# Optimization experiments

Hardware: AMD Instinct MI355X
Metric: run time of the kernel (lower is better)

The kernel has to match this reference:

```python
import jax, jax.numpy as jnp
import numpy as np

D_MODEL = 1024
N_HEADS = 16
D_K = D_MODEL // N_HEADS
SIGMA = 1.0
NUM_ITERS = 3
PAD_POS = 10000.0


def setup_inputs() -> dict:
    rng = jax.random.key(0)
    ks = jax.random.split(rng, 16)
    B, Lq, Lk = 8, 512, 512
    s = 1.0 / np.sqrt(D_MODEL).astype(np.float32)
    return {
        "query": jax.random.normal(ks[0], (B, Lq, D_MODEL), jnp.float32),
        "key": jax.random.normal(ks[1], (B, Lk, D_MODEL), jnp.float32),
        "value": jax.random.normal(ks[2], (B, Lk, D_MODEL), jnp.float32),
        "query_lengths": jax.random.randint(ks[3], (B,), 2, Lq),
        "key_lengths": jax.random.randint(ks[4], (B,), 2, Lk),
        "Wq": jax.random.normal(ks[5], (D_MODEL, D_MODEL), jnp.float32) * s,
        "bq": jnp.zeros((D_MODEL,), jnp.float32),
        "Wk": jax.random.normal(ks[6], (D_MODEL, D_MODEL), jnp.float32) * s,
        "bk": jnp.zeros((D_MODEL,), jnp.float32),
        "Wv": jax.random.normal(ks[7], (D_MODEL, D_MODEL), jnp.float32) * s,
        "bv": jnp.zeros((D_MODEL,), jnp.float32),
        "Wo": jax.random.normal(ks[8], (D_MODEL, D_MODEL), jnp.float32) * s,
        "bo": jnp.zeros((D_MODEL,), jnp.float32),
        "pos_scale": jnp.ones((1,), jnp.float32),
        "pos_bias": jnp.zeros((1,), jnp.float32),
    }


def _init_positions(lengths, max_len, scale, bias):
    # vectorized tcr_pep init: linspace(-L/2, L/2, L) per row, pad -> 10000
    j = jnp.arange(max_len, dtype=jnp.float32)[None, :]          # [1, L]
    L = lengths.astype(jnp.float32)[:, None]                      # [B, 1]
    step = jnp.where(L > 1.0, L / (L - 1.0), 0.0)                 # linspace step
    pos = (-L / 2.0 + j * step) * scale + bias
    pad = jnp.arange(max_len)[None, :] >= lengths[:, None]
    return jnp.where(pad, PAD_POS, pos)


def _distance_attention(qp, kp):
    d2 = (qp[:, :, None] - kp[:, None, :]) ** 2                   # [B, Lq, Lk]
    attn = jnp.exp(-d2 / (2.0 * SIGMA * SIGMA))
    masked = (qp[:, :, None] >= 1000.0) | (kp[:, None, :] >= 1000.0)
    return jnp.where(masked, 0.0, attn)


def _update_positions(qp, kp, attn):
    qn = attn / jnp.clip(attn.sum(-1, keepdims=True), 1e-9)
    qp_new = jnp.einsum('bqk,bk->bq', qn, kp)
    at = attn.transpose(0, 2, 1)
    kn = at / jnp.clip(at.sum(-1, keepdims=True), 1e-9)
    kp_new = jnp.einsum('bkq,bq->bk', kn, qp)
    qp_new = jnp.where(qp >= 1000.0, PAD_POS, qp_new)
    kp_new = jnp.where(kp >= 1000.0, PAD_POS, kp_new)
    return qp_new, kp_new


def reference(query, key, value, query_lengths, key_lengths,
              Wq, bq, Wk, bk, Wv, bv, Wo, bo, pos_scale, pos_bias):
    B, Lq, _ = query.shape
    Lk = key.shape[1]

    def split_heads(x):
        return x.reshape(B, -1, N_HEADS, D_K).transpose(0, 2, 1, 3)  # [B,H,L,Dk]

    q = split_heads(query @ Wq.T + bq)
    k = split_heads(key @ Wk.T + bk)
    v = split_heads(value @ Wv.T + bv)

    qp = _init_positions(query_lengths, Lq, pos_scale, pos_bias)  # [B, Lq]
    kp = _init_positions(key_lengths, Lk, pos_scale, pos_bias)    # [B, Lk]

    scores = jnp.einsum('bhqd,bhkd->bhqk', q, k) / jnp.sqrt(jnp.float32(D_K))
    attn = jax.nn.softmax(scores, axis=-1)                        # [B,H,Lq,Lk]

    for _ in range(NUM_ITERS):
        da = _distance_attention(qp, kp)                          # [B,Lq,Lk]
        comb = attn * da[:, None, :, :]
        comb = comb / jnp.clip(comb.sum(-1, keepdims=True), 1e-9)
        qp, kp = _update_positions(qp, kp, da)
        attn = comb

    ctx = jnp.einsum('bhqk,bhkd->bhqd', attn, v)
    ctx = ctx.transpose(0, 2, 1, 3).reshape(B, Lq, D_MODEL)
    out = ctx @ Wo.T + bo
    return out, attn.mean(axis=1)
```

## Files before the change

kernel.cpp:

```cpp
#include <hip/hip_runtime.h>
#include <math.h>

#define B_  8
#define LQ  512
#define LK  512
#define DM  1024
#define NH  16
#define DK  64
constexpr float PADP = 10000.0f;

typedef short s16x8 __attribute__((ext_vector_type(8)));
typedef float f32x4 __attribute__((ext_vector_type(4)));

__device__ inline unsigned short f2b1(float f) {
    unsigned u = __float_as_uint(f);
    unsigned r = (u + 0x7fffu + ((u >> 16) & 1u)) >> 16;
    return (unsigned short)r;
}
__device__ inline float b2f1(unsigned short h) {
    return __uint_as_float(((unsigned)h) << 16);
}

__global__ __launch_bounds__(256) void f2b_all_kernel(
    const float* __restrict__ query, const float* __restrict__ key,
    const float* __restrict__ value,
    const float* __restrict__ Wq, const float* __restrict__ Wk,
    const float* __restrict__ Wv, const float* __restrict__ Wo,
    unsigned short* __restrict__ xq, unsigned short* __restrict__ xk,
    unsigned short* __restrict__ xv,
    unsigned short* __restrict__ wqb, unsigned short* __restrict__ wkb,
    unsigned short* __restrict__ wvb, unsigned short* __restrict__ wob)
{
    const int s = blockIdx.y;
    const float* src;
    unsigned short* dst;
    if (s < 4)       { src = query + ((size_t)s << 20);       dst = xq + ((size_t)s << 20); }
    else if (s < 8)  { src = key   + ((size_t)(s - 4) << 20); dst = xk + ((size_t)(s - 4) << 20); }
    else if (s < 12) { src = value + ((size_t)(s - 8) << 20); dst = xv + ((size_t)(s - 8) << 20); }
    else {
        const int w = s - 12;
        src = (w == 0) ? Wq : (w == 1) ? Wk : (w == 2) ? Wv : Wo;
        dst = (w == 0) ? wqb : (w == 1) ? wkb : (w == 2) ? wvb : wob;
    }
    const int i = blockIdx.x * 256 + threadIdx.x;
    const float4 v = *(const float4*)&src[(size_t)i * 4];
    ushort4 o;
    o.x = f2b1(v.x); o.y = f2b1(v.y); o.z = f2b1(v.z); o.w = f2b1(v.w);
    *(ushort4*)&dst[(size_t)i * 4] = o;
}

template <int PHASE>
__global__ __launch_bounds__(512) void daRow_kernel(
    const int* __restrict__ qlen, const int* __restrict__ klen,
    const float* __restrict__ pscale, const float* __restrict__ pbias,
    float* __restrict__ posQ,
    const float* __restrict__ posKin, float* __restrict__ posKout,
    const float* __restrict__ rsIn, const float* __restrict__ rdIn,
    const float* __restrict__ colSIn, const float* __restrict__ colDIn,
    float* __restrict__ rsOut, float* __restrict__ rdOut,
    float* __restrict__ colSOut, float* __restrict__ colDOut,
    unsigned short* __restrict__ Dplane)
{
    constexpr int NCH = 16, QC = LQ / NCH;
    __shared__ float kpl[LK];
    __shared__ float csp[8][LK], cdp[8][LK];
    const int chunk = blockIdx.x, b = blockIdx.y;
    const int t = threadIdx.x, w = t >> 6, lane = t & 63;

    float scale = 0.0f, bias = 0.0f;
    if (PHASE == 0) { scale = pscale[0]; bias = pbias[0]; }

    if (PHASE == 0) {
        const int kl = klen[b];
        const float Lf = (float)kl;
        const float step = (Lf > 1.0f) ? Lf / (Lf - 1.0f) : 0.0f;
        const float pos = (-Lf * 0.5f + (float)t * step) * scale + bias;
        const float kv = (t >= kl) ? PADP : pos;
        kpl[t] = kv;
        if (chunk == 0) posKout[b * LK + t] = kv;
    } else {
        float colsum = 0.0f, coldot = 0.0f;
#pragma unroll
        for (int c = 0; c < NCH; ++c) {
            colsum += colSIn[((size_t)b * NCH + c) * LK + t];
            coldot += colDIn[((size_t)b * NCH + c) * LK + t];
        }
        const float prev = posKin[b * LK + t];
        const float kv = (prev >= 1000.0f) ? PADP : coldot / fmaxf(colsum, 1e-9f);
        kpl[t] = kv;
        if (PHASE == 1 && chunk == 0) posKout[b * LK + t] = kv;
    }
    __syncthreads();

    float cs[8] = {0,0,0,0,0,0,0,0}, cd[8] = {0,0,0,0,0,0,0,0};
    unsigned short* Dbb = Dplane + (size_t)b * LQ * LK;

    for (int qi = chunk * QC + w; qi < chunk * QC + QC; qi += 8) {
        float qpv;
        if (PHASE == 0) {
            const int ql = qlen[b];
            const float Lf = (float)ql;
            const float step = (Lf > 1.0f) ? Lf / (Lf - 1.0f) : 0.0f;
            qpv = (qi >= ql) ? PADP : (-Lf * 0.5f + (float)qi * step) * scale + bias;
            if (lane == 0) posQ[b * LQ + qi] = qpv;
        } else {
            const float prev = posQ[b * LQ + qi];
            qpv = (prev >= 1000.0f) ? PADP
                : rdIn[b * LQ + qi] / fmaxf(rsIn[b * LQ + qi], 1e-9f);
            if (PHASE == 1 && lane == 0) posQ[b * LQ + qi] = qpv;
        }
        const bool qpad = (qpv >= 1000.0f);
        float rsum = 0.0f, rdot = 0.0f;
#pragma unroll
        for (int c = 0; c < 8; ++c) {
            const int k = lane + 64 * c;
            const float kpv = kpl[k];
            const float d = qpv - kpv;
            float e = (qpad || (kpv >= 1000.0f)) ? 0.0f : __expf(-0.5f * d * d);
            if (PHASE < 2) { rsum += e; rdot += e * kpv; cs[c] += e; cd[c] += e * qpv; }
            Dbb[(size_t)qi * LK + k] = f2b1(e);
        }
        if (PHASE < 2) {
#pragma unroll
            for (int o = 32; o > 0; o >>= 1) {
                rsum += __shfl_xor(rsum, o);
                rdot += __shfl_xor(rdot, o);
            }
            if (lane == 0) { rsOut[b * LQ + qi] = rsum; rdOut[b * LQ + qi] = rdot; }
        }
    }
    if (PHASE < 2) {
#pragma unroll
        for (int c = 0; c < 8; ++c) {
            csp[w][lane + 64 * c] = cs[c];
            cdp[w][lane + 64 * c] = cd[c];
        }
        __syncthreads();
        float s = 0.0f, dd = 0.0f;
        for (int ww = 0; ww < 8; ++ww) { s += csp[ww][t]; dd += cdp[ww][t]; }
        colSOut[((size_t)b * NCH + chunk) * LK + t] = s;
        colDOut[((size_t)b * NCH + chunk) * LK + t] = dd;
    }
}

__global__ __launch_bounds__(256) void transpose_bf16(
    const unsigned short* __restrict__ in, unsigned short* __restrict__ out,
    int Mn, int Nn)
{
    __shared__ unsigned short tile[64][65];
    const int m0 = blockIdx.y * 64, n0 = blockIdx.x * 64;
    const int t = threadIdx.x;
    const int r = t >> 3, c8 = (t & 7) * 8;
#pragma unroll
    for (int rr = 0; rr < 64; rr += 32) {
        const uint4 v = *(const uint4*)&in[(size_t)(m0 + r + rr) * Nn + n0 + c8];
        const unsigned short* pv = (const unsigned short*)&v;
#pragma unroll
        for (int j = 0; j < 8; ++j) tile[r + rr][c8 + j] = pv[j];
    }
    __syncthreads();
#pragma unroll
    for (int rr = 0; rr < 64; rr += 32) {
        unsigned short tmp[8];
#pragma unroll
        for (int j = 0; j < 8; ++j) tmp[j] = tile[c8 + j][r + rr];
        *(uint4*)&out[(size_t)(n0 + r + rr) * Mn + m0 + c8] = *(uint4*)tmp;
    }
}

template <bool OB>
__global__ __launch_bounds__(256) void gemm_bf16_nt(
    const unsigned short* __restrict__ A,
    const unsigned short* __restrict__ Bt,
    void* __restrict__ Cv,
    const float* __restrict__ bias,
    int M, int N, int K)
{
    __shared__ short As[64 * 32];
    __shared__ short Bs[128 * 32];
    const int m0 = blockIdx.y * 64, n0 = blockIdx.x * 128;
    const int t = threadIdx.x;
    const int wid = t >> 6, lane = t & 63;
    const int wr = wid >> 1, wc = wid & 1;
    const int lr = lane & 15, lk = (lane >> 4) * 8;

    f32x4 acc[2][4] = {};

    const int srow = lane >> 2;
    const int scol = (lane & 3) * 8;

    for (int kb = 0; kb < K; kb += 32) {
        __syncthreads();
        {
            const unsigned short* g = &A[(size_t)(m0 + wid * 16 + srow) * K + kb + scol];
            __builtin_amdgcn_global_load_lds((const unsigned*)g,
                (unsigned*)&As[(wid * 16) * 32], 16, 0, 0);
        }
#pragma unroll
        for (int u = 0; u < 2; ++u) {
            const unsigned short* g = &Bt[(size_t)(n0 + wid * 32 + u * 16 + srow) * K + kb + scol];
            __builtin_amdgcn_global_load_lds((const unsigned*)g,
                (unsigned*)&Bs[(wid * 32 + u * 16) * 32], 16, 0, 0);
        }
        __syncthreads();

        s16x8 af[2], bf[4];
#pragma unroll
        for (int i = 0; i < 2; ++i)
            af[i] = *(const s16x8*)&As[(wr * 32 + i * 16 + lr) * 32 + lk];
#pragma unroll
        for (int j = 0; j < 4; ++j)
            bf[j] = *(const s16x8*)&Bs[(wc * 64 + j * 16 + lr) * 32 + lk];
#pragma unroll
        for (int i = 0; i < 2; ++i)
#pragma unroll
            for (int j = 0; j < 4; ++j)
                acc[i][j] = __builtin_amdgcn_mfma_f32_16x16x32_bf16(
                    af[i], bf[j], acc[i][j], 0, 0, 0);
    }

    const int r0 = (lane >> 4) * 4;
#pragma unroll
    for (int i = 0; i < 2; ++i) {
        const int row = m0 + wr * 32 + i * 16 + r0;
#pragma unroll
        for (int j = 0; j < 4; ++j) {
            const int col = n0 + wc * 64 + j * 16 + lr;
            const float bvv = bias ? bias[col] : 0.0f;
#pragma unroll
            for (int r = 0; r < 4; ++r) {
                const float val = acc[i][j][r] + bvv;
                if (OB) ((unsigned short*)Cv)[(size_t)(row + r) * N + col] = f2b1(val);
                else    ((float*)Cv)[(size_t)(row + r) * N + col] = val;
            }
        }
    }
}

__global__ __launch_bounds__(512) void attn_fused(
    const unsigned short* __restrict__ Qb,
    const unsigned short* __restrict__ Kb,
    const unsigned short* __restrict__ D,
    unsigned short* __restrict__ Ab)
{
    constexpr int KP = 72;
    constexpr int SP = 520;
    __shared__ short pool[64 * SP];
    __shared__ float red[8][64];
    short* Qs = pool;
    short* Ks = pool + 4608;

    const int z = blockIdx.y;
    const int b = z >> 4, h = z & 15;
    const int q0 = blockIdx.x * 64;
    const int t = threadIdx.x;
    const int wid = t >> 6, lane = t & 63;
    const int lr = lane & 15, lkq = (lane >> 4) * 8;
    const int rbase = (lane >> 4) * 4;

    {
        const int row = t >> 3, seg = (t & 7) * 8;
        *(uint4*)&Qs[row * KP + seg] =
            *(const uint4*)&Qb[((size_t)(b * LQ + q0 + row)) * DM + h * DK + seg];
    }

    f32x4 acc[2][4][2] = {};

#pragma unroll
    for (int kh = 0; kh < 2; ++kh) {
        __syncthreads();
        {
            const int row = t >> 1, seg = (t & 1) * 32;
            const unsigned short* src =
                &Kb[((size_t)(b * LK + kh * 256 + row)) * DM + h * DK + seg];
#pragma unroll
            for (int s = 0; s < 4; ++s)
                *(uint4*)&Ks[row * KP + seg + s * 8] = *(const uint4*)(src + s * 8);
        }
        __syncthreads();

#pragma unroll
        for (int ks = 0; ks < 2; ++ks) {
            s16x8 af[4], bf[2];
#pragma unroll
            for (int i = 0; i < 4; ++i)
                af[i] = *(const s16x8*)&Qs[(i * 16 + lr) * KP + ks * 32 + lkq];
#pragma unroll
            for (int j = 0; j < 2; ++j)
                bf[j] = *(const s16x8*)&Ks[(wid * 32 + j * 16 + lr) * KP + ks * 32 + lkq];
#pragma unroll
            for (int i = 0; i < 4; ++i)
#pragma unroll
                for (int j = 0; j < 2; ++j)
                    acc[kh][i][j] = __builtin_amdgcn_mfma_f32_16x16x32_bf16(
                        af[i], bf[j], acc[kh][i][j], 0, 0, 0);
        }
    }

    float M[4][4];
#pragma unroll
    for (int i = 0; i < 4; ++i)
#pragma unroll
        for (int r = 0; r < 4; ++r) {
            float m = acc[0][i][0][r];
            m = fmaxf(m, acc[0][i][1][r]);
            m = fmaxf(m, acc[1][i][0][r]);
            m = fmaxf(m, acc[1][i][1][r]);
#pragma unroll
            for (int o = 1; o < 16; o <<= 1)
                m = fmaxf(m, __shfl_xor(m, o));
            M[i][r] = m;
        }
    __syncthreads();
    if (lr == 0) {
#pragma unroll
        for (int i = 0; i < 4; ++i)
#pragma unroll
            for (int r = 0; r < 4; ++r)
                red[wid][i * 16 + rbase + r] = M[i][r];
    }
    __syncthreads();
#pragma unroll
    for (int i = 0; i < 4; ++i)
#pragma unroll
        for (int r = 0; r < 4; ++r) {
            float m = red[0][i * 16 + rbase + r];
#pragma unroll
            for (int ww = 1; ww < 8; ++ww)
                m = fmaxf(m, red[ww][i * 16 + rbase + r]);
            M[i][r] = m;
        }

#pragma unroll
    for (int kh = 0; kh < 2; ++kh)
#pragma unroll
        for (int i = 0; i < 4; ++i)
#pragma unroll
            for (int j = 0; j < 2; ++j) {
                const int col = kh * 256 + wid * 32 + j * 16 + lr;
#pragma unroll
                for (int r = 0; r < 4; ++r) {
                    const int row = i * 16 + rbase + r;
                    const float e = __expf((acc[kh][i][j][r] - M[i][r]) * 0.125f);
                    pool[row * SP + col] = (short)f2b1(e);
                }
            }
    __syncthreads();

    for (int rr = wid * 8; rr < wid * 8 + 8; ++rr) {
        float v[8];
        {
            const uint4 ev = *(const uint4*)&pool[rr * SP + lane * 8];
            const unsigned short* pe = (const unsigned short*)&ev;
#pragma unroll
            for (int j = 0; j < 8; ++j) v[j] = b2f1(pe[j]);
        }
        float s = 0.0f;
#pragma unroll
        for (int j = 0; j < 8; ++j) s += v[j];
#pragma unroll
        for (int o = 32; o > 0; o >>= 1) s += __shfl_xor(s, o);
        const float invz = 1.0f / s;
#pragma unroll
        for (int j = 0; j < 8; ++j) v[j] *= invz;

#pragma unroll
        for (int it = 0; it < 3; ++it) {
            const uint4 dv = *(const uint4*)&D[
                (((size_t)it * B_ + b) * LQ + q0 + rr) * LK + lane * 8];
            const unsigned short* pd = (const unsigned short*)&dv;
            float s2 = 0.0f;
#pragma unroll
            for (int j = 0; j < 8; ++j) {
                v[j] *= b2f1(pd[j]);
                s2 += v[j];
            }
#pragma unroll
            for (int o = 32; o > 0; o >>= 1) s2 += __shfl_xor(s2, o);
            const float inv = 1.0f / fmaxf(s2, 1e-9f);
#pragma unroll
            for (int j = 0; j < 8; ++j) v[j] *= inv;
        }

        ushort4 u0, u1;
        u0.x = f2b1(v[0]); u0.y = f2b1(v[1]); u0.z = f2b1(v[2]); u0.w = f2b1(v[3]);
        u1.x = f2b1(v[4]); u1.y = f2b1(v[5]); u1.z = f2b1(v[6]); u1.w = f2b1(v[7]);
        unsigned short* arow = Ab + ((size_t)z * LQ + q0 + rr) * LK + lane * 8;
        *(ushort4*)&arow[0] = u0;
        *(ushort4*)&arow[4] = u1;
    }
}

__global__ __launch_bounds__(256) void meanB_kernel(
    const unsigned short* __restrict__ Ab, float* __restrict__ meanOut)
{
    const int b = blockIdx.x >> 9, q = blockIdx.x & 511;
    const int t = threadIdx.x;
    const int c0 = t * 2;
    float s0 = 0.0f, s1 = 0.0f;
#pragma unroll
    for (int h = 0; h < 16; ++h) {
        const unsigned short* row = Ab + (((size_t)(b * 16 + h)) * LQ + q) * LK;
        const unsigned v = *(const unsigned*)&row[c0];
        s0 += b2f1((unsigned short)(v & 0xffff));
        s1 += b2f1((unsigned short)(v >> 16));
    }
    float* o = meanOut + ((size_t)b * LQ + q) * LK + c0;
    o[0] = s0 * (1.0f / 16.0f);
    o[1] = s1 * (1.0f / 16.0f);
}

__global__ __launch_bounds__(256) void ctx_mfma(
    const unsigned short* __restrict__ Ab,
    const unsigned short* __restrict__ VbT,
    unsigned short* __restrict__ ctxb)
{
    constexpr int BKP = 72;
    __shared__ short As[64 * BKP];
    __shared__ short Bs[64 * BKP];
    const int z = blockIdx.z;
    const int b = z >> 4, h = z & 15;
    const int hcol = h * DK;
    const int q0 = blockIdx.y * 64;
    const int t = threadIdx.x;
    const int wid = t >> 6, lane = t & 63;
    const int wr = wid >> 1, wc = wid & 1;
    const int lr = lane & 15, lk = (lane >> 4) * 8;

    const unsigned short* Abase = Ab + ((size_t)z * LQ + q0) * LK;
    const unsigned short* Bbase = VbT + (size_t)hcol * (B_ * LK) + (size_t)b * LK;

    f32x4 acc[2][2] = {};
    const int srow = t >> 2, sseg = (t & 3) * 16;

    for (int kb = 0; kb < LK; kb += 64) {
        const uint4 a0 = *(const uint4*)&Abase[(size_t)srow * LK + kb + sseg];
        const uint4 a1 = *(const uint4*)&Abase[(size_t)srow * LK + kb + sseg + 8];
        const uint4 b0 = *(const uint4*)&Bbase[(size_t)srow * (B_ * LK) + kb + sseg];
        const uint4 b1 = *(const uint4*)&Bbase[(size_t)srow * (B_ * LK) + kb + sseg + 8];
        __syncthreads();
        *(uint4*)&As[srow * BKP + sseg] = a0;
        *(uint4*)&As[srow * BKP + sseg + 8] = a1;
        *(uint4*)&Bs[srow * BKP + sseg] = b0;
        *(uint4*)&Bs[srow * BKP + sseg + 8] = b1;
        __syncthreads();

#pragma unroll
        for (int kh = 0; kh < 2; ++kh) {
            s16x8 af[2], bf[2];
#pragma unroll
            for (int i = 0; i < 2; ++i)
                af[i] = *(const s16x8*)&As[(wr * 32 + i * 16 + lr) * BKP + kh * 32 + lk];
#pragma unroll
            for (int j = 0; j < 2; ++j)
                bf[j] = *(const s16x8*)&Bs[(wc * 32 + j * 16 + lr) * BKP + kh * 32 + lk];
#pragma unroll
            for (int i = 0; i < 2; ++i)
#pragma unroll
                for (int j = 0; j < 2; ++j)
                    acc[i][j] = __builtin_amdgcn_mfma_f32_16x16x32_bf16(
                        af[i], bf[j], acc[i][j], 0, 0, 0);
        }
    }

    const int r0 = (lane >> 4) * 4;
#pragma unroll
    for (int i = 0; i < 2; ++i) {
        const int row = b * LQ + q0 + wr * 32 + i * 16 + r0;
#pragma unroll
        for (int j = 0; j < 2; ++j) {
            const int col = hcol + wc * 32 + j * 16 + lr;
#pragma unroll
            for (int r = 0; r < 4; ++r)
                ctxb[(size_t)(row + r) * DM + col] = f2b1(acc[i][j][r]);
        }
    }
}

template <bool BT>
__global__ __launch_bounds__(256) void gemm64(
    const float* __restrict__ A, int lda, long aS1, long aS2,
    const float* __restrict__ Bm, int ldb, long bS1, long bS2,
    float* __restrict__ C, int ldc, long cS1, long cS2,
    const float* __restrict__ bias, int K, float alpha, int zshift)
{
    const int z = blockIdx.z;
    const long z1 = z >> zshift;
    const long z2 = z & ((1 << zshift) - 1);
    A  += z1 * aS1 + z2 * aS2;
    Bm += z1 * bS1 + z2 * bS2;
    C  += z1 * cS1 + z2 * cS2;

    const int m0 = blockIdx.y * 64, n0 = blockIdx.x * 64;
    __shared__ float As[32][68];
    __shared__ float Bs[32][68];
    const int t = threadIdx.x;
    const int ty = t >> 4, tx = t & 15;

    float acc[4][4];
#pragma unroll
    for (int i = 0; i < 4; ++i)
#pragma unroll
        for (int j = 0; j < 4; ++j) acc[i][j] = 0.0f;

    const int mA = t >> 3;
    const int kA = (t & 7) * 4;

    for (int kb = 0; kb < K; kb += 32) {
        {
            const float4 a0 = *(const float4*)&A[(size_t)(m0 + mA) * lda + kb + kA];
            const float4 a1 = *(const float4*)&A[(size_t)(m0 + mA + 32) * lda + kb + kA];
            As[kA + 0][mA] = a0.x; As[kA + 1][mA] = a0.y; As[kA + 2][mA] = a0.z; As[kA + 3][mA] = a0.w;
            As[kA + 0][mA + 32] = a1.x; As[kA + 1][mA + 32] = a1.y; As[kA + 2][mA + 32] = a1.z; As[kA + 3][mA + 32] = a1.w;
        }
        if (BT) {
            const float4 b0 = *(const float4*)&Bm[(size_t)(n0 + mA) * ldb + kb + kA];
            const float4 b1 = *(const float4*)&Bm[(size_t)(n0 + mA + 32) * ldb + kb + kA];
            Bs[kA + 0][mA] = b0.x; Bs[kA + 1][mA] = b0.y; Bs[kA + 2][mA] = b0.z; Bs[kA + 3][mA] = b0.w;
            Bs[kA + 0][mA + 32] = b1.x; Bs[kA + 1][mA + 32] = b1.y; Bs[kA + 2][mA + 32] = b1.z; Bs[kA + 3][mA + 32] = b1.w;
        } else {
            const int kB = t >> 4;
            const int nB = (t & 15) * 4;
            const float4 b0 = *(const float4*)&Bm[(size_t)(kb + kB) * ldb + n0 + nB];
            const float4 b1 = *(const float4*)&Bm[(size_t)(kb + kB + 16) * ldb + n0 + nB];
            *(float4*)&Bs[kB][nB] = b0;
            *(float4*)&Bs[kB + 16][nB] = b1;
        }
        __syncthreads();

#pragma unroll
        for (int kk = 0; kk < 32; ++kk) {
            const float4 av = *(const float4*)&As[kk][ty * 4];
            const float4 bv = *(const float4*)&Bs[kk][tx * 4];
            const float a[4] = {av.x, av.y, av.z, av.w};
            const float bb[4] = {bv.x, bv.y, bv.z, bv.w};
#pragma unroll
            for (int i = 0; i < 4; ++i)
#pragma unroll
                for (int j = 0; j < 4; ++j)
                    acc[i][j] = fmaf(a[i], bb[j], acc[i][j]);
        }
        __syncthreads();
    }

#pragma unroll
    for (int i = 0; i < 4; ++i) {
        const int row = m0 + ty * 4 + i;
        float4 o;
        o.x = acc[i][0] * alpha;
        o.y = acc[i][1] * alpha;
        o.z = acc[i][2] * alpha;
        o.w = acc[i][3] * alpha;
        if (bias) {
            o.x += bias[n0 + tx * 4 + 0];
            o.y += bias[n0 + tx * 4 + 1];
            o.z += bias[n0 + tx * 4 + 2];
            o.w += bias[n0 + tx * 4 + 3];
        }
        *(float4*)&C[(size_t)row * ldc + n0 + tx * 4] = o;
    }
}

template <bool BF16OUT>
__global__ __launch_bounds__(256) void softmaxP_kernel(
    float* __restrict__ S, const unsigned short* __restrict__ D,
    void* __restrict__ AOut, float* __restrict__ meanOut,
    int nheads, int accumulate)
{
    const int b = blockIdx.x >> 9, q = blockIdx.x & 511;
    const int t = threadIdx.x, w = t >> 6, lane = t & 63;
    __shared__ float Pl[3][LK];
    __shared__ float part[4][LK];
    const size_t NPB = (size_t)B_ * LQ * LK;
    const size_t rowoff = ((size_t)b * LQ + q) * LK;

    for (int i = t; i < LK; i += 256) {
        Pl[0][i] = b2f1(D[rowoff + i]);
        Pl[1][i] = b2f1(D[NPB + rowoff + i]);
        Pl[2][i] = b2f1(D[2 * NPB + rowoff + i]);
    }
    __syncthreads();

    float macc[8];
#pragma unroll
    for (int j = 0; j < 8; ++j) macc[j] = 0.0f;

    for (int h = w; h < nheads; h += 4) {
        const size_t roff = (((size_t)b * nheads + h) * LQ + q) * LK;
        const float* row = S + roff;
        float v[8];
        const float4 s0 = *(const float4*)&row[lane * 8];
        const float4 s1 = *(const float4*)&row[lane * 8 + 4];
        v[0] = s0.x; v[1] = s0.y; v[2] = s0.z; v[3] = s0.w;
        v[4] = s1.x; v[5] = s1.y; v[6] = s1.z; v[7] = s1.w;
        float mx = v[0];
#pragma unroll
        for (int j = 1; j < 8; ++j) mx = fmaxf(mx, v[j]);
#pragma unroll
        for (int o = 32; o > 0; o >>= 1) mx = fmaxf(mx, __shfl_xor(mx, o));
        float zz = 0.0f;
#pragma unroll
        for (int j = 0; j < 8; ++j) { v[j] = __expf(v[j] - mx); zz += v[j]; }
#pragma unroll
        for (int o = 32; o > 0; o >>= 1) zz += __shfl_xor(zz, o);
        const float invz = 1.0f / zz;
#pragma unroll
        for (int j = 0; j < 8; ++j) v[j] *= invz;

#pragma unroll
        for (int it = 0; it < 3; ++it) {
            float s = 0.0f;
#pragma unroll
            for (int j = 0; j < 8; ++j) {
                v[j] *= Pl[it][lane * 8 + j];
                s += v[j];
            }
#pragma unroll
            for (int o = 32; o > 0; o >>= 1) s += __shfl_xor(s, o);
            const float inv = 1.0f / fmaxf(s, 1e-9f);
#pragma unroll
            for (int j = 0; j < 8; ++j) v[j] *= inv;
        }

#pragma unroll
        for (int j = 0; j < 8; ++j) macc[j] += v[j];

        if (BF16OUT) {
            unsigned short* arow = (unsigned short*)AOut + roff;
            ushort4 u0, u1;
            u0.x = f2b1(v[0]); u0.y = f2b1(v[1]); u0.z = f2b1(v[2]); u0.w = f2b1(v[3]);
            u1.x = f2b1(v[4]); u1.y = f2b1(v[5]); u1.z = f2b1(v[6]); u1.w = f2b1(v[7]);
            *(ushort4*)&arow[lane * 8] = u0;
            *(ushort4*)&arow[lane * 8 + 4] = u1;
        } else {
            float* arow = (float*)AOut + roff;
            *(float4*)&arow[lane * 8] = make_float4(v[0], v[1], v[2], v[3]);
            *(float4*)&arow[lane * 8 + 4] = make_float4(v[4], v[5], v[6], v[7]);
        }
    }

    *(float4*)&part[w][lane * 8] = make_float4(macc[0], macc[1], macc[2], macc[3]);
    *(float4*)&part[w][lane * 8 + 4] = make_float4(macc[4], macc[5], macc[6], macc[7]);
    __syncthreads();

    for (int i = t; i < LK; i += 256) {
        const float m = (part[0][i] + part[1][i] + part[2][i] + part[3][i]) * (1.0f / 16.0f);
        const size_t oi = ((size_t)b * LQ + q) * LK + i;
        meanOut[oi] = accumulate ? (meanOut[oi] + m) : m;
    }
}

extern "C" void kernel_launch(void* const* d_in, const int* in_sizes, int n_in,
                              void* d_out, int out_size, void* d_ws, size_t ws_size,
                              hipStream_t stream)
{
    const float* query  = (const float*)d_in[0];
    const float* key    = (const float*)d_in[1];
    const float* value  = (const float*)d_in[2];
    const int*   qlen   = (const int*)d_in[3];
    const int*   klen   = (const int*)d_in[4];
    const float* Wq     = (const float*)d_in[5];
    const float* bq     = (const float*)d_in[6];
    const float* Wk     = (const float*)d_in[7];
    const float* bk     = (const float*)d_in[8];
    const float* Wv     = (const float*)d_in[9];
    const float* bv     = (const float*)d_in[10];
    const float* Wo     = (const float*)d_in[11];
    const float* bo     = (const float*)d_in[12];
    const float* pscale = (const float*)d_in[13];
    const float* pbias  = (const float*)d_in[14];

    float* out     = (float*)d_out;
    float* meanOut = out + (size_t)B_ * LQ * DM;

    const size_t NQKV = (size_t)B_ * LQ * DM;
    const size_t NP   = (size_t)B_ * LQ * LK;
    const size_t NW   = (size_t)DM * DM;
    const size_t NS   = (size_t)B_ * NH * LQ * LK;
    const size_t NPOS = (size_t)B_ * LQ;
    const size_t NCOL = (size_t)B_ * 16 * LK;

    unsigned short* Dbuf = (unsigned short*)d_ws;
    float* posQ  = (float*)(Dbuf + 3 * NP);
    float* posK1 = posQ + NPOS;
    float* posK2 = posK1 + NPOS;
    float* rs1   = posK2 + NPOS;
    float* rd1   = rs1 + NPOS;
    float* rs2   = rd1 + NPOS;
    float* rd2   = rs2 + NPOS;
    float* colS1 = rd2 + NPOS;
    float* colD1 = colS1 + NCOL;
    float* colS2 = colD1 + NCOL;
    float* colD2 = colS2 + NCOL;
    float* fend  = colD2 + NCOL;
    unsigned short* Qb   = (unsigned short*)fend;
    unsigned short* Kb   = Qb + NQKV;
    unsigned short* Vb   = Kb + NQKV;
    unsigned short* VbT  = Vb + NQKV;
    unsigned short* ctxb = VbT + NQKV;
    unsigned short* wqb  = ctxb + NQKV;
    unsigned short* wkb  = wqb + NW;
    unsigned short* wvb  = wkb + NW;
    unsigned short* wob  = wvb + NW;
    unsigned short* Ab   = wob + NW;
    unsigned short* xq = Ab;
    unsigned short* xk = xq + NQKV;
    unsigned short* xv = xk + NQKV;

    const size_t need_full = (size_t)((char*)(Ab + NS) - (char*)d_ws);

    if (ws_size >= need_full) {
        dim3 gDa(16, B_);
        daRow_kernel<0><<<gDa, 512, 0, stream>>>(qlen, klen, pscale, pbias,
            posQ, nullptr, posK1,
            nullptr, nullptr, nullptr, nullptr,
            rs1, rd1, colS1, colD1, Dbuf);
        daRow_kernel<1><<<gDa, 512, 0, stream>>>(qlen, klen, pscale, pbias,
            posQ, posK1, posK2,
            rs1, rd1, colS1, colD1,
            rs2, rd2, colS2, colD2, Dbuf + NP);
        daRow_kernel<2><<<gDa, 512, 0, stream>>>(qlen, klen, pscale, pbias,
            posQ, posK2, nullptr,
            rs2, rd2, colS2, colD2,
            nullptr, nullptr, nullptr, nullptr, Dbuf + 2 * NP);

        dim3 gF(1024, 16);
        f2b_all_kernel<<<gF, 256, 0, stream>>>(query, key, value, Wq, Wk, Wv, Wo,
                                               xq, xk, xv, wqb, wkb, wvb, wob);

        dim3 gP(DM / 128, (B_ * LQ) / 64);
        gemm_bf16_nt<true><<<gP, 256, 0, stream>>>(xq, wqb, Qb, bq, B_ * LQ, DM, DM);
        gemm_bf16_nt<true><<<gP, 256, 0, stream>>>(xk, wkb, Kb, bk, B_ * LQ, DM, DM);
        gemm_bf16_nt<true><<<gP, 256, 0, stream>>>(xv, wvb, Vb, bv, B_ * LQ, DM, DM);

        dim3 gT(DM / 64, (B_ * LK) / 64);
        transpose_bf16<<<gT, 256, 0, stream>>>(Vb, VbT, B_ * LK, DM);

        dim3 gA(LQ / 64, B_ * NH);
        attn_fused<<<gA, 512, 0, stream>>>(Qb, Kb, Dbuf, Ab);

        meanB_kernel<<<B_ * LQ, 256, 0, stream>>>(Ab, meanOut);

        dim3 gC(1, LQ / 64, B_ * NH);
        ctx_mfma<<<gC, 256, 0, stream>>>(Ab, VbT, ctxb);

        gemm_bf16_nt<false><<<gP, 256, 0, stream>>>(ctxb, wob, out, bo, B_ * LQ, DM, DM);
        return;
    }

    float* qbuf = (float*)d_ws;
    float* kbuf = qbuf + NQKV;
    float* vbuf = kbuf + NQKV;
    unsigned short* Dfb = (unsigned short*)(vbuf + NQKV);
    float* Sfb  = (float*)(Dfb + 3 * NP);
    float* ctxbuf = Sfb + NP;
    float* pQ  = ctxbuf + NQKV;
    float* pK1 = pQ + NPOS;
    float* pK2 = pK1 + NPOS;
    float* frs1 = pK2 + NPOS;
    float* frd1 = frs1 + NPOS;
    float* frs2 = frd1 + NPOS;
    float* frd2 = frs2 + NPOS;
    float* fcS1 = frd2 + NPOS;
    float* fcD1 = fcS1 + NCOL;
    float* fcS2 = fcD1 + NCOL;
    float* fcD2 = fcS2 + NCOL;

    dim3 gDa(16, B_);
    daRow_kernel<0><<<gDa, 512, 0, stream>>>(qlen, klen, pscale, pbias,
        pQ, nullptr, pK1, nullptr, nullptr, nullptr, nullptr,
        frs1, frd1, fcS1, fcD1, Dfb);
    daRow_kernel<1><<<gDa, 512, 0, stream>>>(qlen, klen, pscale, pbias,
        pQ, pK1, pK2, frs1, frd1, fcS1, fcD1,
        frs2, frd2, fcS2, fcD2, Dfb + NP);
    daRow_kernel<2><<<gDa, 512, 0, stream>>>(qlen, klen, pscale, pbias,
        pQ, pK2, nullptr, frs2, frd2, fcS2, fcD2,
        nullptr, nullptr, nullptr, nullptr, Dfb + 2 * NP);

    dim3 gProj(DM / 64, (B_ * LQ) / 64, 1);
    gemm64<true><<<gProj, 256, 0, stream>>>(query, DM, 0, 0, Wq, DM, 0, 0,
                                            qbuf, DM, 0, 0, bq, DM, 1.0f, 0);
    gemm64<true><<<gProj, 256, 0, stream>>>(key, DM, 0, 0, Wk, DM, 0, 0,
                                            kbuf, DM, 0, 0, bk, DM, 1.0f, 0);
    gemm64<true><<<gProj, 256, 0, stream>>>(value, DM, 0, 0, Wv, DM, 0, 0,
                                            vbuf, DM, 0, 0, bv, DM, 1.0f, 0);
    for (int h = 0; h < NH; ++h) {
        dim3 gS2(LK / 64, LQ / 64, B_);
        gemm64<true><<<gS2, 256, 0, stream>>>(
            qbuf + h * DK, DM, (long)LQ * DM, 0,
            kbuf + h * DK, DM, (long)LK * DM, 0,
            Sfb, LK, (long)LQ * LK, 0,
            nullptr, DK, 0.125f, 0);
        softmaxP_kernel<false><<<B_ * LQ, 256, 0, stream>>>(Sfb, Dfb, Sfb, meanOut, 1, h > 0 ? 1 : 0);
        dim3 gC2(1, LQ / 64, B_);
        gemm64<false><<<gC2, 256, 0, stream>>>(
            Sfb, LK, (long)LQ * LK, 0,
            vbuf + h * DK, DM, (long)LK * DM, 0,
            ctxbuf + h * DK, DM, (long)LQ * DM, 0,
            nullptr, LK, 1.0f, 0);
    }
    dim3 gO(DM / 64, (B_ * LQ) / 64, 1);
    gemm64<true><<<gO, 256, 0, stream>>>(ctxbuf, DM, 0, 0, Wo, DM, 0, 0,
                                         out, DM, 0, 0, bo, DM, 1.0f, 0);
}
```

Baseline: 217.6 us.

## Split attention block into two 32-row halves to halve LDS and accumulators

The fused attention kernel now handles its 64 query rows as two sequential 32-row halves. K is streamed in four 128-row chunks instead of two 256-row chunks, and the shared pool and reduction buffers shrink by half. The aim is to cut LDS use and accumulator registers per block so more blocks fit on each CU and occupancy rises. In exchange, K is loaded from global memory twice per block and the kernel needs more barriers.

```diff
diff --git a/kernel.cpp b/kernel.cpp
--- a/kernel.cpp
+++ b/kernel.cpp
@@ -245,10 +245,10 @@
 {
     constexpr int KP = 72;
     constexpr int SP = 520;
-    __shared__ short pool[64 * SP];
-    __shared__ float red[8][64];
+    __shared__ short pool[32 * SP];
+    __shared__ float red[8][32];
     short* Qs = pool;
-    short* Ks = pool + 4608;
+    short* Ks = pool + 2304;
 
     const int z = blockIdx.y;
     const int b = z >> 4, h = z & 15;
@@ -258,136 +258,131 @@
     const int lr = lane & 15, lkq = (lane >> 4) * 8;
     const int rbase = (lane >> 4) * 4;
 
-    {
-        const int row = t >> 3, seg = (t & 7) * 8;
-        *(uint4*)&Qs[row * KP + seg] =
-            *(const uint4*)&Qb[((size_t)(b * LQ + q0 + row)) * DM + h * DK + seg];
-    }
-
-    f32x4 acc[2][4][2] = {};
-
-#pragma unroll
-    for (int kh = 0; kh < 2; ++kh) {
+    for (int hb = 0; hb < 2; ++hb) {
+        if (hb) __syncthreads();
+
+        {
+            const int row = t >> 4, seg = (t & 15) * 4;
+            *(uint2*)&Qs[row * KP + seg] = *(const uint2*)
+                &Qb[((size_t)(b * LQ + q0 + hb * 32 + row)) * DM + h * DK + seg];
+        }
+
+        f32x4 acc[4][2] = {};
+
+        for (int kq = 0; kq < 4; ++kq) {
+            __syncthreads();
+            {
+                const int row = t >> 2, seg = (t & 3) * 16;
+                const unsigned short* src =
+                    &Kb[((size_t)(b * LK + kq * 128 + row)) * DM + h * DK + seg];
+                *(uint4*)&Ks[row * KP + seg]     = *(const uint4*)(src);
+                *(uint4*)&Ks[row * KP + seg + 8] = *(const uint4*)(src + 8);
+            }
+            __syncthreads();
+#pragma unroll
+            for (int ks = 0; ks < 2; ++ks) {
+                s16x8 af[2], bf;
+#pragma unroll
+                for (int ii = 0; ii < 2; ++ii)
+                    af[ii] = *(const s16x8*)&Qs[(ii * 16 + lr) * KP + ks * 32 + lkq];
+                bf = *(const s16x8*)&Ks[(wid * 16 + lr) * KP + ks * 32 + lkq];
+#pragma unroll
+                for (int ii = 0; ii < 2; ++ii)
+                    acc[kq][ii] = __builtin_amdgcn_mfma_f32_16x16x32_bf16(
+                        af[ii], bf, acc[kq][ii], 0, 0, 0);
+            }
+        }
+
+        float M[2][4];
+#pragma unroll
+        for (int ii = 0; ii < 2; ++ii)
+#pragma unroll
+            for (int r = 0; r < 4; ++r) {
+                float m = acc[0][ii][r];
+                m = fmaxf(m, acc[1][ii][r]);
+                m = fmaxf(m, acc[2][ii][r]);
+                m = fmaxf(m, acc[3][ii][r]);
+#pragma unroll
+                for (int o = 1; o < 16; o <<= 1)
+                    m = fmaxf(m, __shfl_xor(m, o));
+                M[ii][r] = m;
+            }
+        if (lr == 0) {
+#pragma unroll
+            for (int ii = 0; ii < 2; ++ii)
+#pragma unroll
+                for (int r = 0; r < 4; ++r)
+                    red[wid][ii * 16 + rbase + r] = M[ii][r];
+        }
         __syncthreads();
-        {
-            const int row = t >> 1, seg = (t & 1) * 32;
-            const unsigned short* src =
-                &Kb[((size_t)(b * LK + kh * 256 + row)) * DM + h * DK + seg];
-#pragma unroll
-            for (int s = 0; s < 4; ++s)
-                *(uint4*)&Ks[row * KP + seg + s * 8] = *(const uint4*)(src + s * 8);
-        }
+#pragma unroll
+        for (int ii = 0; ii < 2; ++ii)
+#pragma unroll
+            for (int r = 0; r < 4; ++r) {
+                float m = red[0][ii * 16 + rbase + r];
+#pragma unroll
+                for (int ww = 1; ww < 8; ++ww)
+                    m = fmaxf(m, red[ww][ii * 16 + rbase + r]);
+                M[ii][r] = m;
+            }
+
+#pragma unroll
+        for (int ii = 0; ii < 2; ++ii)
+#pragma unroll
+            for (int kq = 0; kq < 4; ++kq) {
+                const int col = kq * 128 + wid * 16 + lr;
+#pragma unroll
+                for (int r = 0; r < 4; ++r) {
+                    const int lrow = ii * 16 + rbase + r;
+                    pool[lrow * SP + col] =
+                        (short)f2b1(__expf((acc[kq][ii][r] - M[ii][r]) * 0.125f));
+                }
+            }
         __syncthreads();
 
-#pragma unroll
-        for (int ks = 0; ks < 2; ++ks) {
-            s16x8 af[4], bf[2];
-#pragma unroll
-            for (int i = 0; i < 4; ++i)
-                af[i] = *(const s16x8*)&Qs[(i * 16 + lr) * KP + ks * 32 + lkq];
-#pragma unroll
-            for (int j = 0; j < 2; ++j)
-                bf[j] = *(const s16x8*)&Ks[(wid * 32 + j * 16 + lr) * KP + ks * 32 + lkq];
-#pragma unroll
-            for (int i = 0; i < 4; ++i)
-#pragma unroll
-                for (int j = 0; j < 2; ++j)
-                    acc[kh][i][j] = __builtin_amdgcn_mfma_f32_16x16x32_bf16(
-                        af[i], bf[j], acc[kh][i][j], 0, 0, 0);
-        }
-    }
-
-    float M[4][4];
-#pragma unroll
-    for (int i = 0; i < 4; ++i)
-#pragma unroll
-        for (int r = 0; r < 4; ++r) {
-            float m = acc[0][i][0][r];
-            m = fmaxf(m, acc[0][i][1][r]);
-            m = fmaxf(m, acc[1][i][0][r]);
-            m = fmaxf(m, acc[1][i][1][r]);
-#pragma unroll
-            for (int o = 1; o < 16; o <<= 1)
-                m = fmaxf(m, __shfl_xor(m, o));
-            M[i][r] = m;
-        }
-    __syncthreads();
-    if (lr == 0) {
-#pragma unroll
-        for (int i = 0; i < 4; ++i)
-#pragma unroll
-            for (int r = 0; r < 4; ++r)
-                red[wid][i * 16 + rbase + r] = M[i][r];
-    }
-    __syncthreads();
-#pragma unroll
-    for (int i = 0; i < 4; ++i)
-#pragma unroll
-        for (int r = 0; r < 4; ++r) {
-            float m = red[0][i * 16 + rbase + r];
-#pragma unroll
-            for (int ww = 1; ww < 8; ++ww)
-                m = fmaxf(m, red[ww][i * 16 + rbase + r]);
-            M[i][r] = m;
-        }
-
-#pragma unroll
-    for (int kh = 0; kh < 2; ++kh)
-#pragma unroll
-        for (int i = 0; i < 4; ++i)
-#pragma unroll
-            for (int j = 0; j < 2; ++j) {
-                const int col = kh * 256 + wid * 32 + j * 16 + lr;
-#pragma unroll
-                for (int r = 0; r < 4; ++r) {
-                    const int row = i * 16 + rbase + r;
-                    const float e = __expf((acc[kh][i][j][r] - M[i][r]) * 0.125f);
-                    pool[row * SP + col] = (short)f2b1(e);
+        for (int rl = wid * 4; rl < wid * 4 + 4; ++rl) {
+            const int rr = hb * 32 + rl;
+            float v[8];
+            {
+                const uint4 ev = *(const uint4*)&pool[rl * SP + lane * 8];
+                const unsigned short* pe = (const unsigned short*)&ev;
+#pragma unroll
+                for (int j = 0; j < 8; ++j) v[j] = b2f1(pe[j]);
+            }
+            float s = 0.0f;
+#pragma unroll
+            for (int j = 0; j < 8; ++j) s += v[j];
+#pragma unroll
+            for (int o = 32; o > 0; o >>= 1) s += __shfl_xor(s, o);
+            const float invz = 1.0f / s;
+#pragma unroll
+            for (int j = 0; j < 8; ++j) v[j] *= invz;
+
+#pragma unroll
+            for (int it = 0; it < 3; ++it) {
+                const uint4 dv = *(const uint4*)&D[
+                    (((size_t)it * B_ + b) * LQ + q0 + rr) * LK + lane * 8];
+                const unsigned short* pd = (const unsigned short*)&dv;
+                float s2 = 0.0f;
+#pragma unroll
+                for (int j = 0; j < 8; ++j) {
+                    v[j] *= b2f1(pd[j]);
+                    s2 += v[j];
                 }
-            }
-    __syncthreads();
-
-    for (int rr = wid * 8; rr < wid * 8 + 8; ++rr) {
-        float v[8];
-        {
-            const uint4 ev = *(const uint4*)&pool[rr * SP + lane * 8];
-            const unsigned short* pe = (const unsigned short*)&ev;
-#pragma unroll
-            for (int j = 0; j < 8; ++j) v[j] = b2f1(pe[j]);
-        }
-        float s = 0.0f;
-#pragma unroll
-        for (int j = 0; j < 8; ++j) s += v[j];
-#pragma unroll
-        for (int o = 32; o > 0; o >>= 1) s += __shfl_xor(s, o);
-        const float invz = 1.0f / s;
-#pragma unroll
-        for (int j = 0; j < 8; ++j) v[j] *= invz;
-
-#pragma unroll
-        for (int it = 0; it < 3; ++it) {
-            const uint4 dv = *(const uint4*)&D[
-                (((size_t)it * B_ + b) * LQ + q0 + rr) * LK + lane * 8];
-            const unsigned short* pd = (const unsigned short*)&dv;
-            float s2 = 0.0f;
-#pragma unroll
-            for (int j = 0; j < 8; ++j) {
-                v[j] *= b2f1(pd[j]);
-                s2 += v[j];
-            }
-#pragma unroll
-            for (int o = 32; o > 0; o >>= 1) s2 += __shfl_xor(s2, o);
-            const float inv = 1.0f / fmaxf(s2, 1e-9f);
-#pragma unroll
-            for (int j = 0; j < 8; ++j) v[j] *= inv;
-        }
-
-        ushort4 u0, u1;
-        u0.x = f2b1(v[0]); u0.y = f2b1(v[1]); u0.z = f2b1(v[2]); u0.w = f2b1(v[3]);
-        u1.x = f2b1(v[4]); u1.y = f2b1(v[5]); u1.z = f2b1(v[6]); u1.w = f2b1(v[7]);
-        unsigned short* arow = Ab + ((size_t)z * LQ + q0 + rr) * LK + lane * 8;
-        *(ushort4*)&arow[0] = u0;
-        *(ushort4*)&arow[4] = u1;
+#pragma unroll
+                for (int o = 32; o > 0; o >>= 1) s2 += __shfl_xor(s2, o);
+                const float inv = 1.0f / fmaxf(s2, 1e-9f);
+#pragma unroll
+                for (int j = 0; j < 8; ++j) v[j] *= inv;
+            }
+
+            ushort4 u0, u1;
+            u0.x = f2b1(v[0]); u0.y = f2b1(v[1]); u0.z = f2b1(v[2]); u0.w = f2b1(v[3]);
+            u1.x = f2b1(v[4]); u1.y = f2b1(v[5]); u1.z = f2b1(v[6]); u1.w = f2b1(v[7]);
+            unsigned short* arow = Ab + ((size_t)z * LQ + q0 + rr) * LK + lane * 8;
+            *(ushort4*)&arow[0] = u0;
+            *(ushort4*)&arow[4] = u1;
+        }
     }
 }
 
```

New measurement: 223.1 us. 2.6% more time.
